# Kernel optimization log

Hardware: AMD Instinct MI355X
Metric: run time of the kernel (lower is better)

Reference implementation:

```python
import jax, jax.numpy as jnp
import numpy as np

N_NODES = 50000
N_EDGES = 1600000
IN_CH = 128
HID = 32
HEADS = 2
OUT_CH = 128
N_GRAPHS = 64
NEG_SLOPE = 0.2


def setup_inputs() -> dict:
    key = jax.random.key(0)
    ks = jax.random.split(key, 12)
    x = jax.random.normal(ks[0], (N_NODES, IN_CH), dtype=jnp.float32)
    edge_index = jax.random.randint(ks[1], (2, N_EDGES), 0, N_NODES, dtype=jnp.int64)
    batch = jnp.sort(jax.random.randint(ks[2], (N_NODES,), 0, N_GRAPHS, dtype=jnp.int64))
    s = 0.1
    return {
        "x": x,
        "edge_index": edge_index,
        "batch": batch,
        # conv1: GATConv(IN_CH, 32, heads=2), concat=True -> out 64
        "W1": jax.random.normal(ks[3], (IN_CH, HEADS * HID), dtype=jnp.float32) * s,
        "att_src1": jax.random.normal(ks[4], (HEADS, HID), dtype=jnp.float32) * s,
        "att_dst1": jax.random.normal(ks[5], (HEADS, HID), dtype=jnp.float32) * s,
        "b1": jnp.zeros((HEADS * HID,), dtype=jnp.float32),
        # conv2: GATConv(64, OUT_CH, heads=1)
        "W2": jax.random.normal(ks[6], (HEADS * HID, OUT_CH), dtype=jnp.float32) * s,
        "att_src2": jax.random.normal(ks[7], (1, OUT_CH), dtype=jnp.float32) * s,
        "att_dst2": jax.random.normal(ks[8], (1, OUT_CH), dtype=jnp.float32) * s,
        "b2": jnp.zeros((OUT_CH,), dtype=jnp.float32),
    }


def gat_conv(x, src, dst, W, att_src, att_dst, bias, heads, out_dim):
    """PyG GATConv: edges src->dst, softmax over incoming edges per dst node."""
    n = x.shape[0]
    xl = (x @ W).reshape(n, heads, out_dim)                 # [N,H,D]
    a_s = jnp.sum(xl * att_src, axis=-1)                    # [N,H]
    a_d = jnp.sum(xl * att_dst, axis=-1)                    # [N,H]
    e = jax.nn.leaky_relu(a_s[src] + a_d[dst], NEG_SLOPE)   # [E,H]
    e_max = jax.lax.stop_gradient(jax.ops.segment_max(e, dst, num_segments=n))
    ex = jnp.exp(e - e_max[dst])
    denom = jax.ops.segment_sum(ex, dst, num_segments=n)
    alpha = ex / denom[dst]                                 # [E,H]
    msg = xl[src] * alpha[:, :, None]                       # [E,H,D]
    out = jax.ops.segment_sum(msg, dst, num_segments=n)     # [N,H,D]
    return out.reshape(n, heads * out_dim) + bias


def reference(x, edge_index, batch, W1, att_src1, att_dst1, b1, W2, att_src2, att_dst2, b2):
    n = x.shape[0]
    loop = jnp.arange(n, dtype=edge_index.dtype)
    src = jnp.concatenate([edge_index[0], loop])  # add_self_loops (PyG default)
    dst = jnp.concatenate([edge_index[1], loop])
    h = gat_conv(x, src, dst, W1, att_src1, att_dst1, b1, HEADS, HID)
    h = jax.nn.elu(h)
    h = gat_conv(h, src, dst, W2, att_src2, att_dst2, b2, 1, OUT_CH)
    h = jax.nn.elu(h)
    # global_mean_pool
    sums = jax.ops.segment_sum(h, batch, num_segments=N_GRAPHS)
    cnts = jax.ops.segment_sum(jnp.ones((n,), dtype=h.dtype), batch, num_segments=N_GRAPHS)
    return sums / jnp.maximum(cnts, 1.0)[:, None]
```

## Files before the change

kernel.cpp:

```cpp
#include <hip/hip_runtime.h>

#define N_NODES 50000
#define N_EDGES 1600000
#define E_TOT   (N_EDGES + N_NODES)
#define IN_CH   128
#define C1      64
#define OUT_CH  128
#define N_GRAPHS 64
#define NEG_SLOPE 0.2f

#define BSH   7
#define NBUCK ((N_NODES + 127) / 128)
#define BCAP  5120
#define CHUNK 8192
#define PN    32

typedef __attribute__((ext_vector_type(8))) short bf16x8;
typedef __attribute__((ext_vector_type(4))) float f32x4;
typedef __attribute__((ext_vector_type(2))) float f32x2;

__device__ __forceinline__ float elu_f(float v) {
    return v > 0.f ? v : (__expf(v) - 1.f);
}
__device__ __forceinline__ unsigned short f2bf(float f) {
    unsigned u = __float_as_uint(f);
    return (unsigned short)((u + 0x7FFFu + ((u >> 16) & 1u)) >> 16);
}
__device__ __forceinline__ float bf_lo(unsigned u) { return __uint_as_float(u << 16); }
__device__ __forceinline__ float bf_hi(unsigned u) { return __uint_as_float(u & 0xFFFF0000u); }
__device__ __forceinline__ unsigned char f2fp8(float v) {
    return (unsigned char)(__builtin_amdgcn_cvt_pk_fp8_f32(v, v, 0, false) & 0xFF);
}

__global__ __launch_bounds__(256) void k_gemm1(
    const float* __restrict__ x, const float* __restrict__ W1,
    const float* __restrict__ att_s, const float* __restrict__ att_d,
    unsigned short* __restrict__ xl1, float* __restrict__ a_s, float* __restrict__ a_d)
{
    __shared__ unsigned short W1T[64][136];
    __shared__ float psA[4][16], psD[4][16];
    const int t = threadIdx.x, wave = t >> 6, lane = t & 63;
    const int quad = lane >> 4, lm = lane & 15;
    for (int i = t; i < 128 * 64; i += 256)
        W1T[i & 63][i >> 6] = f2bf(W1[i]);
    __syncthreads();

    const int n0 = wave * 16;
    const int c  = n0 + lm;
    bf16x8 bfr[4];
    #pragma unroll
    for (int s = 0; s < 4; ++s)
        bfr[s] = *(const bf16x8*)&W1T[c][s * 32 + quad * 8];
    const float asc = att_s[c], adc = att_d[c];

    const int r0 = blockIdx.x * 16;
    f32x4 acc = {0.f, 0.f, 0.f, 0.f};
    #pragma unroll
    for (int s = 0; s < 4; ++s) {
        const float* xp = &x[(size_t)(r0 + lm) * 128 + s * 32 + quad * 8];
        float4 xa = *(const float4*)xp;
        float4 xb = *(const float4*)(xp + 4);
        bf16x8 afr;
        afr[0] = (short)f2bf(xa.x); afr[1] = (short)f2bf(xa.y);
        afr[2] = (short)f2bf(xa.z); afr[3] = (short)f2bf(xa.w);
        afr[4] = (short)f2bf(xb.x); afr[5] = (short)f2bf(xb.y);
        afr[6] = (short)f2bf(xb.z); afr[7] = (short)f2bf(xb.w);
        acc = __builtin_amdgcn_mfma_f32_16x16x32_bf16(afr, bfr[s], acc, 0, 0, 0);
    }
    float psv[4], pdv[4];
    #pragma unroll
    for (int r = 0; r < 4; ++r) {
        float v = acc[r];
        xl1[(size_t)(r0 + quad * 4 + r) * 64 + c] = f2bf(v);
        psv[r] = v * asc;
        pdv[r] = v * adc;
    }
    #pragma unroll
    for (int ofs = 1; ofs <= 8; ofs <<= 1) {
        #pragma unroll
        for (int r = 0; r < 4; ++r) {
            psv[r] += __shfl_xor(psv[r], ofs, 64);
            pdv[r] += __shfl_xor(pdv[r], ofs, 64);
        }
    }
    if (lm == 0) {
        #pragma unroll
        for (int r = 0; r < 4; ++r) {
            psA[wave][quad * 4 + r] = psv[r];
            psD[wave][quad * 4 + r] = pdv[r];
        }
    }
    __syncthreads();
    if (t < 32) {
        const int row = t & 15, h = t >> 4;
        a_s[(size_t)(r0 + row) * 2 + h] = psA[2 * h][row] + psA[2 * h + 1][row];
        a_d[(size_t)(r0 + row) * 2 + h] = psD[2 * h][row] + psD[2 * h + 1][row];
    }
}

__global__ __launch_bounds__(256) void k_bin(
    const int* __restrict__ ei, int* __restrict__ gcur, unsigned* __restrict__ bbuf)
{
    __shared__ int cnt[512];
    __shared__ int base[NBUCK];
    __shared__ int cnt2[NBUCK];
    __shared__ int gpos[NBUCK];
    __shared__ unsigned stage[CHUNK];
    __shared__ unsigned short bof[CHUNK];
    const int t = threadIdx.x;
    const long long e0 = (long long)blockIdx.x * CHUNK;
    const int nE = (int)min((long long)CHUNK, (long long)E_TOT - e0);

    cnt[t] = 0; cnt[t + 256] = 0;
    for (int b = t; b < NBUCK; b += 256) cnt2[b] = 0;
    __syncthreads();

    const int per = CHUNK / 256;
    int myb[per]; unsigned mye[per];
    #pragma unroll
    for (int i = 0; i < per; ++i) {
        int idx = t + 256 * i;
        myb[i] = -1;
        if (idx < nE) {
            long long e = e0 + idx;
            int s, d;
            if (e < N_EDGES) { s = ei[e]; d = ei[N_EDGES + e]; }
            else             { s = d = (int)(e - N_EDGES); }
            myb[i] = d >> BSH;
            mye[i] = ((unsigned)(d & 127) << 17) | (unsigned)s;
            atomicAdd(&cnt[myb[i]], 1);
        }
    }
    __syncthreads();
    for (int ofs = 1; ofs < 512; ofs <<= 1) {
        int v0 = (t >= ofs) ? cnt[t - ofs] : 0;
        int v1 = cnt[t + 256 - ofs];
        __syncthreads();
        cnt[t] += v0; cnt[t + 256] += v1;
        __syncthreads();
    }
    for (int b = t; b < NBUCK; b += 256) {
        base[b] = (b == 0) ? 0 : cnt[b - 1];
        int c = cnt[b] - base[b];
        gpos[b] = (c > 0) ? atomicAdd(&gcur[b], c) : 0;
    }
    __syncthreads();
    #pragma unroll
    for (int i = 0; i < per; ++i) {
        if (myb[i] >= 0) {
            int slot = base[myb[i]] + atomicAdd(&cnt2[myb[i]], 1);
            stage[slot] = mye[i];
            bof[slot] = (unsigned short)myb[i];
        }
    }
    __syncthreads();
    for (int i = t; i < nE; i += 256) {
        int b = bof[i];
        int pos = gpos[b] + (i - base[b]);
        if (pos < BCAP)
            bbuf[(size_t)b * BCAP + pos] = stage[i];
    }
}

__global__ __launch_bounds__(256) void k_bsort(
    const int* __restrict__ gcur, unsigned* __restrict__ bbuf,
    int* __restrict__ beg, int* __restrict__ end,
    const float* __restrict__ a_s1, const float* __restrict__ a_d1,
    float* __restrict__ wb1)
{
    __shared__ unsigned est[BCAP];
    __shared__ unsigned sst[BCAP];
    __shared__ int c[128], lbase[128], c2[128];
    __shared__ float adL[256];
    const int b = blockIdx.x, t = threadIdx.x;
    const int n = min(gcur[b], BCAP);
    unsigned* reg = bbuf + (size_t)b * BCAP;
    for (int i = t; i < n; i += 256) est[i] = reg[i];
    if (t < 128) { c[t] = 0; c2[t] = 0; }
    {
        int dn = (b << BSH) + (t >> 1);
        adL[t] = (dn < N_NODES) ? a_d1[((size_t)b << 8) + t] : 0.f;
    }
    __syncthreads();
    for (int i = t; i < n; i += 256) atomicAdd(&c[est[i] >> 17], 1);
    __syncthreads();
    for (int ofs = 1; ofs < 128; ofs <<= 1) {
        int v = (t < 128 && t >= ofs) ? c[t - ofs] : 0;
        __syncthreads();
        if (t < 128) c[t] += v;
        __syncthreads();
    }
    if (t < 128) {
        lbase[t] = (t == 0) ? 0 : c[t - 1];
        int dst = (b << BSH) + t;
        if (dst < N_NODES) {
            beg[dst] = b * BCAP + lbase[t];
            end[dst] = b * BCAP + c[t];
        }
    }
    __syncthreads();
    for (int i = t; i < n; i += 256) {
        unsigned v = est[i];
        int dl = (int)(v >> 17);
        int pos = lbase[dl] + atomicAdd(&c2[dl], 1);
        sst[pos] = v;
    }
    __syncthreads();
    for (int i = t; i < n; i += 256) {
        unsigned v = sst[i];
        reg[i] = v;
        int s  = (int)(v & 0x1FFFFu);
        int dl = (int)(v >> 17);
        float2 as = *(const float2*)&a_s1[(size_t)s * 2];
        float e0 = as.x + adL[dl * 2];     e0 = e0 > 0.f ? e0 : NEG_SLOPE * e0;
        float e1 = as.y + adL[dl * 2 + 1]; e1 = e1 > 0.f ? e1 : NEG_SLOPE * e1;
        float2 wv; wv.x = __expf(e0); wv.y = __expf(e1);
        *(float2*)&wb1[((size_t)b * BCAP + i) * 2] = wv;
    }
}

#define FMA8(vv, ww) do { \
    acc[0] = fmaf(bf_lo(vv.x), ww, acc[0]); acc[1] = fmaf(bf_hi(vv.x), ww, acc[1]); \
    acc[2] = fmaf(bf_lo(vv.y), ww, acc[2]); acc[3] = fmaf(bf_hi(vv.y), ww, acc[3]); \
    acc[4] = fmaf(bf_lo(vv.z), ww, acc[4]); acc[5] = fmaf(bf_hi(vv.z), ww, acc[5]); \
    acc[6] = fmaf(bf_lo(vv.w), ww, acc[6]); acc[7] = fmaf(bf_hi(vv.w), ww, acc[7]); \
} while (0)

__global__ __launch_bounds__(256) void k_attn1(
    const int* __restrict__ beg_a, const int* __restrict__ end_a,
    const unsigned* __restrict__ csr, const float* __restrict__ wb,
    const unsigned short* __restrict__ xl, const float* __restrict__ b1,
    unsigned short* __restrict__ hout)
{
    const int wave = threadIdx.x >> 6, lane = threadIdx.x & 63;
    const int dst = blockIdx.x * 4 + wave;
    const int beg = beg_a[dst], end = end_a[dst];
    const int li = lane & 7, sub = lane >> 3, hh = li >> 2;

    float acc[8];
    #pragma unroll
    for (int i = 0; i < 8; ++i) acc[i] = 0.f;
    float wsum = 0.f;

    int k = beg;
    for (; k + 32 <= end; k += 32) {
        const int i0 = k + sub;
        const unsigned e0 = csr[i0];
        const unsigned e1 = csr[i0 + 8];
        const unsigned e2 = csr[i0 + 16];
        const unsigned e3 = csr[i0 + 24];
        const float w0 = wb[(size_t)i0 * 2 + hh];
        const float w1 = wb[(size_t)(i0 + 8) * 2 + hh];
        const float w2 = wb[(size_t)(i0 + 16) * 2 + hh];
        const float w3 = wb[(size_t)(i0 + 24) * 2 + hh];
        uint4 v0 = *(const uint4*)&xl[(size_t)(e0 & 0x1FFFFu) * 64 + li * 8];
        uint4 v1 = *(const uint4*)&xl[(size_t)(e1 & 0x1FFFFu) * 64 + li * 8];
        uint4 v2 = *(const uint4*)&xl[(size_t)(e2 & 0x1FFFFu) * 64 + li * 8];
        uint4 v3 = *(const uint4*)&xl[(size_t)(e3 & 0x1FFFFu) * 64 + li * 8];
        wsum += w0 + w1 + w2 + w3;
        FMA8(v0, w0);
        FMA8(v1, w1);
        FMA8(v2, w2);
        FMA8(v3, w3);
    }
    const int last = end - 1;
    for (; k < end; k += 8) {
        const int i0 = k + sub;
        const int c0 = min(i0, last);
        const unsigned e0 = csr[c0];
        float w0 = wb[(size_t)c0 * 2 + hh];
        if (i0 >= end) w0 = 0.f;
        uint4 v0 = *(const uint4*)&xl[(size_t)(e0 & 0x1FFFFu) * 64 + li * 8];
        wsum += w0;
        FMA8(v0, w0);
    }
    #pragma unroll
    for (int ofs = 8; ofs <= 32; ofs <<= 1) {
        wsum += __shfl_xor(wsum, ofs, 64);
        #pragma unroll
        for (int i = 0; i < 8; ++i) acc[i] += __shfl_xor(acc[i], ofs, 64);
    }
    if (sub == 0) {
        const float4 b1a = *(const float4*)&b1[li * 8];
        const float4 b1b = *(const float4*)&b1[li * 8 + 4];
        const float inv = 1.f / wsum;
        float h0 = elu_f(acc[0] * inv + b1a.x);
        float h1 = elu_f(acc[1] * inv + b1a.y);
        float h2 = elu_f(acc[2] * inv + b1a.z);
        float h3 = elu_f(acc[3] * inv + b1a.w);
        float h4 = elu_f(acc[4] * inv + b1b.x);
        float h5 = elu_f(acc[5] * inv + b1b.y);
        float h6 = elu_f(acc[6] * inv + b1b.z);
        float h7 = elu_f(acc[7] * inv + b1b.w);
        uint4 p;
        p.x = (unsigned)f2bf(h0) | ((unsigned)f2bf(h1) << 16);
        p.y = (unsigned)f2bf(h2) | ((unsigned)f2bf(h3) << 16);
        p.z = (unsigned)f2bf(h4) | ((unsigned)f2bf(h5) << 16);
        p.w = (unsigned)f2bf(h6) | ((unsigned)f2bf(h7) << 16);
        *(uint4*)&hout[(size_t)dst * 64 + li * 8] = p;
    }
}

__global__ __launch_bounds__(256) void k_gemm2m(
    const unsigned short* __restrict__ h, const float* __restrict__ W2,
    const float* __restrict__ att_s, const float* __restrict__ att_d,
    unsigned char* __restrict__ xl2, float* __restrict__ a_s, float* __restrict__ a_d)
{
    __shared__ unsigned short W2T[128][72];
    __shared__ float psA[4][16], psD[4][16];
    const int t = threadIdx.x, wave = t >> 6, lane = t & 63;
    const int quad = lane >> 4, lm = lane & 15;
    for (int i = t; i < 64 * 128; i += 256)
        W2T[i & 127][i >> 7] = f2bf(W2[i]);
    __syncthreads();

    const int c0 = wave * 32 + lm;
    const int c1 = c0 + 16;
    bf16x8 bfr0[2], bfr1[2];
    #pragma unroll
    for (int s = 0; s < 2; ++s) {
        bfr0[s] = *(const bf16x8*)&W2T[c0][s * 32 + quad * 8];
        bfr1[s] = *(const bf16x8*)&W2T[c1][s * 32 + quad * 8];
    }
    const float as0 = att_s[c0], as1 = att_s[c1];
    const float ad0 = att_d[c0], ad1 = att_d[c1];

    const int r0 = blockIdx.x * 16;
    f32x4 acc0 = {0.f, 0.f, 0.f, 0.f}, acc1 = {0.f, 0.f, 0.f, 0.f};
    #pragma unroll
    for (int s = 0; s < 2; ++s) {
        bf16x8 afr = *(const bf16x8*)&h[(size_t)(r0 + lm) * 64 + s * 32 + quad * 8];
        acc0 = __builtin_amdgcn_mfma_f32_16x16x32_bf16(afr, bfr0[s], acc0, 0, 0, 0);
        acc1 = __builtin_amdgcn_mfma_f32_16x16x32_bf16(afr, bfr1[s], acc1, 0, 0, 0);
    }
    float psv[4], pdv[4];
    #pragma unroll
    for (int r = 0; r < 4; ++r) {
        float v0 = acc0[r], v1 = acc1[r];
        const size_t row = (size_t)(r0 + quad * 4 + r) * 128;
        xl2[row + c0] = f2fp8(v0);
        xl2[row + c1] = f2fp8(v1);
        psv[r] = v0 * as0 + v1 * as1;
        pdv[r] = v0 * ad0 + v1 * ad1;
    }
    #pragma unroll
    for (int ofs = 1; ofs <= 8; ofs <<= 1) {
        #pragma unroll
        for (int r = 0; r < 4; ++r) {
            psv[r] += __shfl_xor(psv[r], ofs, 64);
            pdv[r] += __shfl_xor(pdv[r], ofs, 64);
        }
    }
    if (lm == 0) {
        #pragma unroll
        for (int r = 0; r < 4; ++r) {
            psA[wave][quad * 4 + r] = psv[r];
            psD[wave][quad * 4 + r] = pdv[r];
        }
    }
    __syncthreads();
    if (t < 16) {
        a_s[r0 + t] = psA[0][t] + psA[1][t] + psA[2][t] + psA[3][t];
        a_d[r0 + t] = psD[0][t] + psD[1][t] + psD[2][t] + psD[3][t];
    }
}

__global__ __launch_bounds__(256) void k_wexp2(
    const int* __restrict__ gcur, const unsigned* __restrict__ bbuf,
    const float* __restrict__ a_s, const float* __restrict__ a_d,
    float* __restrict__ wb2)
{
    const int i = blockIdx.x * 256 + threadIdx.x;
    if (i >= NBUCK * BCAP) return;
    const int b = i / BCAP, pos = i - b * BCAP;
    if (pos >= min(gcur[b], BCAP)) return;
    const unsigned v = bbuf[i];
    const int s = (int)(v & 0x1FFFFu);
    const int d = (b << BSH) | (int)(v >> 17);
    float e = a_s[s] + a_d[d];
    e = e > 0.f ? e : NEG_SLOPE * e;
    wb2[i] = __expf(e);
}

#define CFMA16(vv, ww) do { \
    f32x2 p_; \
    p_ = __builtin_amdgcn_cvt_pk_f32_fp8(vv.x, false); acc[0]  = fmaf(p_.x, ww, acc[0]);  acc[1]  = fmaf(p_.y, ww, acc[1]);  \
    p_ = __builtin_amdgcn_cvt_pk_f32_fp8(vv.x, true);  acc[2]  = fmaf(p_.x, ww, acc[2]);  acc[3]  = fmaf(p_.y, ww, acc[3]);  \
    p_ = __builtin_amdgcn_cvt_pk_f32_fp8(vv.y, false); acc[4]  = fmaf(p_.x, ww, acc[4]);  acc[5]  = fmaf(p_.y, ww, acc[5]);  \
    p_ = __builtin_amdgcn_cvt_pk_f32_fp8(vv.y, true);  acc[6]  = fmaf(p_.x, ww, acc[6]);  acc[7]  = fmaf(p_.y, ww, acc[7]);  \
    p_ = __builtin_amdgcn_cvt_pk_f32_fp8(vv.z, false); acc[8]  = fmaf(p_.x, ww, acc[8]);  acc[9]  = fmaf(p_.y, ww, acc[9]);  \
    p_ = __builtin_amdgcn_cvt_pk_f32_fp8(vv.z, true);  acc[10] = fmaf(p_.x, ww, acc[10]); acc[11] = fmaf(p_.y, ww, acc[11]); \
    p_ = __builtin_amdgcn_cvt_pk_f32_fp8(vv.w, false); acc[12] = fmaf(p_.x, ww, acc[12]); acc[13] = fmaf(p_.y, ww, acc[13]); \
    p_ = __builtin_amdgcn_cvt_pk_f32_fp8(vv.w, true);  acc[14] = fmaf(p_.x, ww, acc[14]); acc[15] = fmaf(p_.y, ww, acc[15]); \
} while (0)

__global__ __launch_bounds__(256) void k_attn2(
    const int* __restrict__ beg_a, const int* __restrict__ end_a,
    const unsigned* __restrict__ csr, const float* __restrict__ wb,
    const unsigned char* __restrict__ xl, float* __restrict__ out)
{
    const int wave = threadIdx.x >> 6, lane = threadIdx.x & 63;
    const int dst = blockIdx.x * 4 + wave;
    const int beg = beg_a[dst], end = end_a[dst];
    const int li = lane & 7, sub = lane >> 3;

    float acc[16];
    #pragma unroll
    for (int i = 0; i < 16; ++i) acc[i] = 0.f;
    float wsum = 0.f;

    int k = beg;
    for (; k + 32 <= end; k += 32) {
        const int i0 = k + sub;
        const unsigned e0 = csr[i0];
        const unsigned e1 = csr[i0 + 8];
        const unsigned e2 = csr[i0 + 16];
        const unsigned e3 = csr[i0 + 24];
        const float w0 = wb[i0];
        const float w1 = wb[i0 + 8];
        const float w2 = wb[i0 + 16];
        const float w3 = wb[i0 + 24];
        uint4 v0 = *(const uint4*)&xl[(size_t)(e0 & 0x1FFFFu) * 128 + li * 16];
        uint4 v1 = *(const uint4*)&xl[(size_t)(e1 & 0x1FFFFu) * 128 + li * 16];
        uint4 v2 = *(const uint4*)&xl[(size_t)(e2 & 0x1FFFFu) * 128 + li * 16];
        uint4 v3 = *(const uint4*)&xl[(size_t)(e3 & 0x1FFFFu) * 128 + li * 16];
        wsum += w0 + w1 + w2 + w3;
        CFMA16(v0, w0);
        CFMA16(v1, w1);
        CFMA16(v2, w2);
        CFMA16(v3, w3);
    }
    const int last = end - 1;
    for (; k < end; k += 8) {
        const int i0 = k + sub;
        const int c0 = min(i0, last);
        const unsigned e0 = csr[c0];
        float w0 = wb[c0];
        if (i0 >= end) w0 = 0.f;
        uint4 v0 = *(const uint4*)&xl[(size_t)(e0 & 0x1FFFFu) * 128 + li * 16];
        wsum += w0;
        CFMA16(v0, w0);
    }
    #pragma unroll
    for (int ofs = 8; ofs <= 32; ofs <<= 1) {
        wsum += __shfl_xor(wsum, ofs, 64);
        #pragma unroll
        for (int i = 0; i < 16; ++i) acc[i] += __shfl_xor(acc[i], ofs, 64);
    }
    if (sub == 0) {
        const float inv = 1.f / wsum;
        float* op = &out[(size_t)dst * 128 + li * 16];
        #pragma unroll
        for (int q = 0; q < 4; ++q) {
            float4 r;
            r.x = acc[q*4+0] * inv; r.y = acc[q*4+1] * inv;
            r.z = acc[q*4+2] * inv; r.w = acc[q*4+3] * inv;
            *(float4*)(op + q * 4) = r;
        }
    }
}

__global__ __launch_bounds__(256) void k_pool(
    const float* __restrict__ out2, const float* __restrict__ b2,
    const int* __restrict__ batch, float* __restrict__ sums, float* __restrict__ cnts)
{
    const int c    = threadIdx.x & 127;
    const int half = threadIdx.x >> 7;
    const int n0   = blockIdx.x * PN;
    const int nb   = n0 + half;
    if (nb >= N_NODES) return;
    const float bc = b2[c];
    float acc = 0.f;
    int cur = batch[nb], cnt = 0;
    for (int i = half; i < PN; i += 2) {
        int n = n0 + i;
        if (n >= N_NODES) break;
        int g = batch[n];
        if (g != cur) {
            atomicAdd(&sums[cur * OUT_CH + c], acc);
            if (c == 0) atomicAdd(&cnts[cur], (float)cnt);
            acc = 0.f; cnt = 0; cur = g;
        }
        acc += elu_f(out2[(size_t)n * OUT_CH + c] + bc);
        cnt++;
    }
    if (cnt > 0) {
        atomicAdd(&sums[cur * OUT_CH + c], acc);
        if (c == 0) atomicAdd(&cnts[cur], (float)cnt);
    }
}

__global__ __launch_bounds__(256) void k_final(
    const float* __restrict__ sums, const float* __restrict__ cnts,
    float* __restrict__ out)
{
    int i = blockIdx.x * 256 + threadIdx.x;
    if (i >= N_GRAPHS * OUT_CH) return;
    out[i] = sums[i] / fmaxf(cnts[i >> 7], 1.f);
}

extern "C" void kernel_launch(void* const* d_in, const int* in_sizes, int n_in,
                              void* d_out, int out_size, void* d_ws, size_t ws_size,
                              hipStream_t stream)
{
    const float* x    = (const float*)d_in[0];
    const int*   ei   = (const int*)d_in[1];
    const int*   batch= (const int*)d_in[2];
    const float* W1   = (const float*)d_in[3];
    const float* as1  = (const float*)d_in[4];
    const float* ad1  = (const float*)d_in[5];
    const float* b1   = (const float*)d_in[6];
    const float* W2   = (const float*)d_in[7];
    const float* as2  = (const float*)d_in[8];
    const float* ad2  = (const float*)d_in[9];
    const float* b2   = (const float*)d_in[10];

    float* ws = (float*)d_ws;
    size_t o = 0;
    unsigned short* xl1b = (unsigned short*)(ws + o); o += (size_t)N_NODES * C1 / 2;
    unsigned short* hbuf = (unsigned short*)(ws + o); o += (size_t)N_NODES * C1 / 2;
    unsigned char*  xl2q = (unsigned char*)(ws + o);  o += (size_t)N_NODES * OUT_CH / 4;
    float*    a_s1 = ws + o; o += (size_t)N_NODES * 2;
    float*    a_d1 = ws + o; o += (size_t)N_NODES * 2;
    float*    a_s2 = ws + o; o += (size_t)N_NODES;
    float*    a_d2 = ws + o; o += (size_t)N_NODES;
    float*    out2 = ws + o; o += (size_t)N_NODES * OUT_CH;
    unsigned* bbuf = (unsigned*)(ws + o); o += (size_t)NBUCK * BCAP;
    float*    wb1  = ws + o; o += (size_t)NBUCK * BCAP * 2;
    float*    wb2  = ws + o; o += (size_t)NBUCK * BCAP;
    int*      beg  = (int*)(ws + o); o += (size_t)N_NODES;
    int*      end  = (int*)(ws + o); o += (size_t)N_NODES;
    size_t zero_start = o;
    int*      gcur = (int*)(ws + o); o += (size_t)NBUCK;
    float*    sums = ws + o;         o += (size_t)N_GRAPHS * OUT_CH;
    float*    cnts = ws + o;         o += (size_t)N_GRAPHS;
    size_t zero_bytes = (o - zero_start) * sizeof(float);
    hipMemsetAsync(ws + zero_start, 0, zero_bytes, stream);

    const int nchunks = (E_TOT + CHUNK - 1) / CHUNK;

    k_gemm1<<<N_NODES / 16, 256, 0, stream>>>(x, W1, as1, ad1, xl1b, a_s1, a_d1);
    k_bin<<<nchunks, 256, 0, stream>>>(ei, gcur, bbuf);
    k_bsort<<<NBUCK, 256, 0, stream>>>(gcur, bbuf, beg, end, a_s1, a_d1, wb1);
    k_attn1<<<N_NODES / 4, 256, 0, stream>>>(beg, end, bbuf, wb1, xl1b, b1, hbuf);
    k_gemm2m<<<(N_NODES + 15) / 16, 256, 0, stream>>>(hbuf, W2, as2, ad2, xl2q, a_s2, a_d2);
    k_wexp2<<<(NBUCK * BCAP + 255) / 256, 256, 0, stream>>>(gcur, bbuf, a_s2, a_d2, wb2);
    k_attn2<<<N_NODES / 4, 256, 0, stream>>>(beg, end, bbuf, wb2, xl2q, out2);
    k_pool<<<(N_NODES + PN - 1) / PN, 256, 0, stream>>>(out2, b2, batch, sums, cnts);
    k_final<<<(N_GRAPHS * OUT_CH + 255) / 256, 256, 0, stream>>>(sums, cnts, (float*)d_out);
}
```

Measured before the change: 273.5 us.

## Compute attention edge weights inline in aggregation kernels, drop precomputed weight buffers

```diff
diff --git a/kernel.cpp b/kernel.cpp
--- a/kernel.cpp
+++ b/kernel.cpp
@@ -30,6 +30,10 @@
 __device__ __forceinline__ float bf_hi(unsigned u) { return __uint_as_float(u & 0xFFFF0000u); }
 __device__ __forceinline__ unsigned char f2fp8(float v) {
     return (unsigned char)(__builtin_amdgcn_cvt_pk_fp8_f32(v, v, 0, false) & 0xFF);
+}
+__device__ __forceinline__ float lrelu_exp(float e) {
+    e = e > 0.f ? e : NEG_SLOPE * e;
+    return __expf(e);
 }
 
 __global__ __launch_bounds__(256) void k_gemm1(
@@ -164,23 +168,16 @@
 
 __global__ __launch_bounds__(256) void k_bsort(
     const int* __restrict__ gcur, unsigned* __restrict__ bbuf,
-    int* __restrict__ beg, int* __restrict__ end,
-    const float* __restrict__ a_s1, const float* __restrict__ a_d1,
-    float* __restrict__ wb1)
+    int* __restrict__ beg, int* __restrict__ end)
 {
     __shared__ unsigned est[BCAP];
     __shared__ unsigned sst[BCAP];
     __shared__ int c[128], lbase[128], c2[128];
-    __shared__ float adL[256];
     const int b = blockIdx.x, t = threadIdx.x;
     const int n = min(gcur[b], BCAP);
     unsigned* reg = bbuf + (size_t)b * BCAP;
     for (int i = t; i < n; i += 256) est[i] = reg[i];
     if (t < 128) { c[t] = 0; c2[t] = 0; }
-    {
-        int dn = (b << BSH) + (t >> 1);
-        adL[t] = (dn < N_NODES) ? a_d1[((size_t)b << 8) + t] : 0.f;
-    }
     __syncthreads();
     for (int i = t; i < n; i += 256) atomicAdd(&c[est[i] >> 17], 1);
     __syncthreads();
@@ -203,20 +200,10 @@
         unsigned v = est[i];
         int dl = (int)(v >> 17);
         int pos = lbase[dl] + atomicAdd(&c2[dl], 1);
-        sst[pos] = v;
-    }
-    __syncthreads();
-    for (int i = t; i < n; i += 256) {
-        unsigned v = sst[i];
-        reg[i] = v;
-        int s  = (int)(v & 0x1FFFFu);
-        int dl = (int)(v >> 17);
-        float2 as = *(const float2*)&a_s1[(size_t)s * 2];
-        float e0 = as.x + adL[dl * 2];     e0 = e0 > 0.f ? e0 : NEG_SLOPE * e0;
-        float e1 = as.y + adL[dl * 2 + 1]; e1 = e1 > 0.f ? e1 : NEG_SLOPE * e1;
-        float2 wv; wv.x = __expf(e0); wv.y = __expf(e1);
-        *(float2*)&wb1[((size_t)b * BCAP + i) * 2] = wv;
-    }
+        sst[pos] = v & 0x1FFFFu;
+    }
+    __syncthreads();
+    for (int i = t; i < n; i += 256) reg[i] = sst[i];
 }
 
 #define FMA8(vv, ww) do { \
@@ -228,7 +215,8 @@
 
 __global__ __launch_bounds__(256) void k_attn1(
     const int* __restrict__ beg_a, const int* __restrict__ end_a,
-    const unsigned* __restrict__ csr, const float* __restrict__ wb,
+    const unsigned* __restrict__ csr,
+    const float* __restrict__ a_s, const float* __restrict__ a_d,
     const unsigned short* __restrict__ xl, const float* __restrict__ b1,
     unsigned short* __restrict__ hout)
 {
@@ -236,6 +224,7 @@
     const int dst = blockIdx.x * 4 + wave;
     const int beg = beg_a[dst], end = end_a[dst];
     const int li = lane & 7, sub = lane >> 3, hh = li >> 2;
+    const float adh = a_d[(size_t)dst * 2 + hh];
 
     float acc[8];
     #pragma unroll
@@ -245,18 +234,18 @@
     int k = beg;
     for (; k + 32 <= end; k += 32) {
         const int i0 = k + sub;
-        const unsigned e0 = csr[i0];
-        const unsigned e1 = csr[i0 + 8];
-        const unsigned e2 = csr[i0 + 16];
-        const unsigned e3 = csr[i0 + 24];
-        const float w0 = wb[(size_t)i0 * 2 + hh];
-        const float w1 = wb[(size_t)(i0 + 8) * 2 + hh];
-        const float w2 = wb[(size_t)(i0 + 16) * 2 + hh];
-        const float w3 = wb[(size_t)(i0 + 24) * 2 + hh];
-        uint4 v0 = *(const uint4*)&xl[(size_t)(e0 & 0x1FFFFu) * 64 + li * 8];
-        uint4 v1 = *(const uint4*)&xl[(size_t)(e1 & 0x1FFFFu) * 64 + li * 8];
-        uint4 v2 = *(const uint4*)&xl[(size_t)(e2 & 0x1FFFFu) * 64 + li * 8];
-        uint4 v3 = *(const uint4*)&xl[(size_t)(e3 & 0x1FFFFu) * 64 + li * 8];
+        const int s0 = (int)csr[i0];
+        const int s1 = (int)csr[i0 + 8];
+        const int s2 = (int)csr[i0 + 16];
+        const int s3 = (int)csr[i0 + 24];
+        const float w0 = lrelu_exp(a_s[(size_t)s0 * 2 + hh] + adh);
+        const float w1 = lrelu_exp(a_s[(size_t)s1 * 2 + hh] + adh);
+        const float w2 = lrelu_exp(a_s[(size_t)s2 * 2 + hh] + adh);
+        const float w3 = lrelu_exp(a_s[(size_t)s3 * 2 + hh] + adh);
+        uint4 v0 = *(const uint4*)&xl[(size_t)s0 * 64 + li * 8];
+        uint4 v1 = *(const uint4*)&xl[(size_t)s1 * 64 + li * 8];
+        uint4 v2 = *(const uint4*)&xl[(size_t)s2 * 64 + li * 8];
+        uint4 v3 = *(const uint4*)&xl[(size_t)s3 * 64 + li * 8];
         wsum += w0 + w1 + w2 + w3;
         FMA8(v0, w0);
         FMA8(v1, w1);
@@ -267,10 +256,10 @@
     for (; k < end; k += 8) {
         const int i0 = k + sub;
         const int c0 = min(i0, last);
-        const unsigned e0 = csr[c0];
-        float w0 = wb[(size_t)c0 * 2 + hh];
+        const int s0 = (int)csr[c0];
+        float w0 = lrelu_exp(a_s[(size_t)s0 * 2 + hh] + adh);
         if (i0 >= end) w0 = 0.f;
-        uint4 v0 = *(const uint4*)&xl[(size_t)(e0 & 0x1FFFFu) * 64 + li * 8];
+        uint4 v0 = *(const uint4*)&xl[(size_t)s0 * 64 + li * 8];
         wsum += w0;
         FMA8(v0, w0);
     }
@@ -365,23 +354,6 @@
     }
 }
 
-__global__ __launch_bounds__(256) void k_wexp2(
-    const int* __restrict__ gcur, const unsigned* __restrict__ bbuf,
-    const float* __restrict__ a_s, const float* __restrict__ a_d,
-    float* __restrict__ wb2)
-{
-    const int i = blockIdx.x * 256 + threadIdx.x;
-    if (i >= NBUCK * BCAP) return;
-    const int b = i / BCAP, pos = i - b * BCAP;
-    if (pos >= min(gcur[b], BCAP)) return;
-    const unsigned v = bbuf[i];
-    const int s = (int)(v & 0x1FFFFu);
-    const int d = (b << BSH) | (int)(v >> 17);
-    float e = a_s[s] + a_d[d];
-    e = e > 0.f ? e : NEG_SLOPE * e;
-    wb2[i] = __expf(e);
-}
-
 #define CFMA16(vv, ww) do { \
     f32x2 p_; \
     p_ = __builtin_amdgcn_cvt_pk_f32_fp8(vv.x, false); acc[0]  = fmaf(p_.x, ww, acc[0]);  acc[1]  = fmaf(p_.y, ww, acc[1]);  \
@@ -396,13 +368,15 @@
 
 __global__ __launch_bounds__(256) void k_attn2(
     const int* __restrict__ beg_a, const int* __restrict__ end_a,
-    const unsigned* __restrict__ csr, const float* __restrict__ wb,
+    const unsigned* __restrict__ csr,
+    const float* __restrict__ a_s, const float* __restrict__ a_d,
     const unsigned char* __restrict__ xl, float* __restrict__ out)
 {
     const int wave = threadIdx.x >> 6, lane = threadIdx.x & 63;
     const int dst = blockIdx.x * 4 + wave;
     const int beg = beg_a[dst], end = end_a[dst];
     const int li = lane & 7, sub = lane >> 3;
+    const float ad0 = a_d[dst];
 
     float acc[16];
     #pragma unroll
@@ -412,18 +386,18 @@
     int k = beg;
     for (; k + 32 <= end; k += 32) {
         const int i0 = k + sub;
-        const unsigned e0 = csr[i0];
-        const unsigned e1 = csr[i0 + 8];
-        const unsigned e2 = csr[i0 + 16];
-        const unsigned e3 = csr[i0 + 24];
-        const float w0 = wb[i0];
-        const float w1 = wb[i0 + 8];
-        const float w2 = wb[i0 + 16];
-        const float w3 = wb[i0 + 24];
-        uint4 v0 = *(const uint4*)&xl[(size_t)(e0 & 0x1FFFFu) * 128 + li * 16];
-        uint4 v1 = *(const uint4*)&xl[(size_t)(e1 & 0x1FFFFu) * 128 + li * 16];
-        uint4 v2 = *(const uint4*)&xl[(size_t)(e2 & 0x1FFFFu) * 128 + li * 16];
-        uint4 v3 = *(const uint4*)&xl[(size_t)(e3 & 0x1FFFFu) * 128 + li * 16];
+        const int s0 = (int)csr[i0];
+        const int s1 = (int)csr[i0 + 8];
+        const int s2 = (int)csr[i0 + 16];
+        const int s3 = (int)csr[i0 + 24];
+        const float w0 = lrelu_exp(a_s[s0] + ad0);
+        const float w1 = lrelu_exp(a_s[s1] + ad0);
+        const float w2 = lrelu_exp(a_s[s2] + ad0);
+        const float w3 = lrelu_exp(a_s[s3] + ad0);
+        uint4 v0 = *(const uint4*)&xl[(size_t)s0 * 128 + li * 16];
+        uint4 v1 = *(const uint4*)&xl[(size_t)s1 * 128 + li * 16];
+        uint4 v2 = *(const uint4*)&xl[(size_t)s2 * 128 + li * 16];
+        uint4 v3 = *(const uint4*)&xl[(size_t)s3 * 128 + li * 16];
         wsum += w0 + w1 + w2 + w3;
         CFMA16(v0, w0);
         CFMA16(v1, w1);
@@ -434,10 +408,10 @@
     for (; k < end; k += 8) {
         const int i0 = k + sub;
         const int c0 = min(i0, last);
-        const unsigned e0 = csr[c0];
-        float w0 = wb[c0];
+        const int s0 = (int)csr[c0];
+        float w0 = lrelu_exp(a_s[s0] + ad0);
         if (i0 >= end) w0 = 0.f;
-        uint4 v0 = *(const uint4*)&xl[(size_t)(e0 & 0x1FFFFu) * 128 + li * 16];
+        uint4 v0 = *(const uint4*)&xl[(size_t)s0 * 128 + li * 16];
         wsum += w0;
         CFMA16(v0, w0);
     }
@@ -526,8 +500,6 @@
     float*    a_d2 = ws + o; o += (size_t)N_NODES;
     float*    out2 = ws + o; o += (size_t)N_NODES * OUT_CH;
     unsigned* bbuf = (unsigned*)(ws + o); o += (size_t)NBUCK * BCAP;
-    float*    wb1  = ws + o; o += (size_t)NBUCK * BCAP * 2;
-    float*    wb2  = ws + o; o += (size_t)NBUCK * BCAP;
     int*      beg  = (int*)(ws + o); o += (size_t)N_NODES;
     int*      end  = (int*)(ws + o); o += (size_t)N_NODES;
     size_t zero_start = o;
@@ -541,11 +513,10 @@
 
     k_gemm1<<<N_NODES / 16, 256, 0, stream>>>(x, W1, as1, ad1, xl1b, a_s1, a_d1);
     k_bin<<<nchunks, 256, 0, stream>>>(ei, gcur, bbuf);
-    k_bsort<<<NBUCK, 256, 0, stream>>>(gcur, bbuf, beg, end, a_s1, a_d1, wb1);
-    k_attn1<<<N_NODES / 4, 256, 0, stream>>>(beg, end, bbuf, wb1, xl1b, b1, hbuf);
+    k_bsort<<<NBUCK, 256, 0, stream>>>(gcur, bbuf, beg, end);
+    k_attn1<<<N_NODES / 4, 256, 0, stream>>>(beg, end, bbuf, a_s1, a_d1, xl1b, b1, hbuf);
     k_gemm2m<<<(N_NODES + 15) / 16, 256, 0, stream>>>(hbuf, W2, as2, ad2, xl2q, a_s2, a_d2);
-    k_wexp2<<<(NBUCK * BCAP + 255) / 256, 256, 0, stream>>>(gcur, bbuf, a_s2, a_d2, wb2);
-    k_attn2<<<N_NODES / 4, 256, 0, stream>>>(beg, end, bbuf, wb2, xl2q, out2);
+    k_attn2<<<N_NODES / 4, 256, 0, stream>>>(beg, end, bbuf, a_s2, a_d2, xl2q, out2);
     k_pool<<<(N_NODES + PN - 1) / PN, 256, 0, stream>>>(out2, b2, batch, sums, cnts);
     k_final<<<(N_GRAPHS * OUT_CH + 255) / 256, 256, 0, stream>>>(sums, cnts, (float*)d_out);
 }
```

New measurement: 259.2 us. 1.05x faster.
